# Performance work log

Hardware: AMD Instinct MI355X
Metric: run time of the kernel (lower is better)

## Reference

```python
import jax, jax.numpy as jnp
import numpy as np

N, E = 50000, 400000
IN, HID, OUT = 256, 192, 128  # hidden = floor((128+256)/2) = 192


def setup_inputs() -> dict:
    key = jax.random.key(0)
    ks = jax.random.split(key, 8)
    def glorot(k, fi, fo):
        lim = (6.0 / (fi + fo)) ** 0.5
        return jax.random.uniform(k, (fi, fo), jnp.float32, -lim, lim)
    return {
        "x": jax.random.normal(ks[0], (N, IN), jnp.float32),
        "edge_index": jax.random.randint(ks[1], (2, E), 0, N, jnp.int64),
        "W1": glorot(ks[2], IN, HID),  "b1": jnp.zeros((HID,), jnp.float32),
        "W2": glorot(ks[3], HID, HID), "b2": jnp.zeros((HID,), jnp.float32),
        "W3": glorot(ks[4], HID, OUT), "b3": jnp.zeros((OUT,), jnp.float32),
    }


def gcn_conv(x, src, dst, norm, W, b, n):
    # PyG GCNConv: out = D^-1/2 (A+I) D^-1/2 (x W) + b
    h = x @ W                               # [N, Fout]
    msg = h[src] * norm[:, None]            # [E+N, Fout] gathered, normalized messages
    return jax.ops.segment_sum(msg, dst, num_segments=n) + b


def reference(x, edge_index, W1, b1, W2, b2, W3, b3):
    n = x.shape[0]
    loops = jnp.arange(n, dtype=edge_index.dtype)
    src = jnp.concatenate([edge_index[0], loops])  # add self-loops
    dst = jnp.concatenate([edge_index[1], loops])
    deg = jax.ops.segment_sum(jnp.ones_like(dst, dtype=x.dtype), dst, num_segments=n)
    dinv = jnp.where(deg > 0, deg ** -0.5, 0.0)
    norm = dinv[src] * dinv[dst]            # [E+N]

    h = jax.nn.relu(gcn_conv(x, src, dst, norm, W1, b1, n))
    h = jax.nn.relu(gcn_conv(h, src, dst, norm, W2, b2, n))
    h = jax.nn.sigmoid(gcn_conv(h, src, dst, norm, W3, b3, n))
    # vectorized replacement of the per-element Python threshold loop
    h_clone = jnp.where(h >= 0.5, 1.0, 0.0).astype(h.dtype)
    return h, h_clone
```

## Files before the change

kernel.cpp:

```cpp
#include <hip/hip_runtime.h>
#include <math.h>

constexpr int Nn   = 50000;
constexpr int Ee   = 400000;
constexpr int FIN  = 256;
constexpr int FHID = 192;
constexpr int FOUT = 128;

typedef float    f32x4 __attribute__((ext_vector_type(4)));
typedef _Float16 f16x8 __attribute__((ext_vector_type(8)));

__device__ inline f32x4 mfma16(f16x8 a, f16x8 b, f32x4 c) {
    return __builtin_amdgcn_mfma_f32_16x16x32_f16(a, b, c, 0, 0, 0);
}


__global__ void init_cnt_k(int* cnt, int n) {
    int i = blockIdx.x * blockDim.x + threadIdx.x;
    if (i < n) cnt[i] = 0;
}

__global__ void detect_k(const long long* p, int n, int* flag) {
    if (threadIdx.x == 0 && blockIdx.x == 0) {
        int ok = 1;
        for (int i = 0; i < 16; i++) {
            long long v = p[i];
            if (v < 0 || v >= n) ok = 0;
        }
        *flag = ok;
    }
}

__global__ void conv_k(const void* edge, const int* flag, int* srcI, int* dstI,
                       int* cnt, int ne) {
    int e = blockIdx.x * blockDim.x + threadIdx.x;
    if (e >= ne) return;
    int s, d;
    if (*flag) {
        const long long* p = (const long long*)edge;
        s = (int)p[e];
        d = (int)p[ne + e];
    } else {
        const int* p = (const int*)edge;
        s = p[e];
        d = p[ne + e];
    }
    srcI[e] = s;
    dstI[e] = d;
    atomicAdd(&cnt[d], 1);
}

__global__ void dinv_k(const int* cnt, float* dinv, int n) {
    int i = blockIdx.x * blockDim.x + threadIdx.x;
    if (i < n) dinv[i] = 1.0f / sqrtf((float)(cnt[i] + 1));
}

__global__ __launch_bounds__(256) void scan1_k(const int* cnt, int n, int* rowptr,
                                               int* blockSum) {
    __shared__ int sm[256];
    int b = blockIdx.x, tid = threadIdx.x;
    int gbase = b * 1024 + tid * 4;
    int v[4];
#pragma unroll
    for (int j = 0; j < 4; j++) v[j] = (gbase + j < n) ? cnt[gbase + j] : 0;
    int tsum = v[0] + v[1] + v[2] + v[3];
    sm[tid] = tsum;
    __syncthreads();
    for (int off = 1; off < 256; off <<= 1) {
        int t = (tid >= off) ? sm[tid - off] : 0;
        __syncthreads();
        sm[tid] += t;
        __syncthreads();
    }
    int excl = sm[tid] - tsum;
#pragma unroll
    for (int j = 0; j < 4; j++) {
        if (gbase + j < n) rowptr[gbase + j] = excl;
        excl += v[j];
    }
    if (tid == 255) blockSum[b] = sm[255];
}

__global__ void scan2_k(const int* blockSum, int nb, int* blockOff) {
    if (threadIdx.x == 0 && blockIdx.x == 0) {
        int run = 0;
        for (int b = 0; b < nb; b++) { blockOff[b] = run; run += blockSum[b]; }
        blockOff[nb] = run;
    }
}

__global__ void scan3_k(int* rowptr, const int* blockOff, int* cursor, int n, int nb) {
    int i = blockIdx.x * blockDim.x + threadIdx.x;
    if (i < n) {
        int r = rowptr[i] + blockOff[i >> 10];
        rowptr[i] = r;
        cursor[i] = r;
    }
    if (i == 0) rowptr[n] = blockOff[nb];
}

__global__ void place_k(const int* srcI, const int* dstI, const float* dinv,
                        int* cursor, int* esrc, float* enorm, int ne) {
    int e = blockIdx.x * blockDim.x + threadIdx.x;
    if (e >= ne) return;
    int s = srcI[e], d = dstI[e];
    int pos = atomicAdd(&cursor[d], 1);
    esrc[pos] = s;
    enorm[pos] = dinv[s] * dinv[d];
}

__global__ void split_w_k(const float* __restrict__ W, _Float16* __restrict__ wh,
                          _Float16* __restrict__ wl, int K, int F) {
    int idx = blockIdx.x * blockDim.x + threadIdx.x;
    if (idx >= K * F) return;
    int k = idx / F, f = idx - k * F;
    float w = W[idx];
    _Float16 h = (_Float16)w;
    float d = w - (float)h;
    wh[(size_t)f * K + k] = h;
    wl[(size_t)f * K + k] = (_Float16)(d * 4096.f);
}

template <int NR, int MODE>
struct KSet {
    f16x8  bh[NR], bl[NR];
    f16x8  ah[2], al[2];
    float4 ar[2][2];
};

template <int K, int F, int NR, int MODE>
__device__ inline void load_set(KSet<NR, MODE>& S, int kk,
                                const float* __restrict__ inF,
                                const _Float16* __restrict__ inH,
                                const _Float16* __restrict__ inL,
                                const _Float16* __restrict__ whi,
                                const _Float16* __restrict__ wlo,
                                int r0, int r1, int cb, int l15) {
#pragma unroll
    for (int ni = 0; ni < NR; ni++) {
        const size_t boff = (size_t)(cb + ni * 16 + l15) * K + kk;
        S.bh[ni] = *(const f16x8*)(whi + boff);
        S.bl[ni] = *(const f16x8*)(wlo + boff);
    }
    if constexpr (MODE == 0) {
        const float* p0 = inF + (size_t)r0 * K + kk;
        const float* p1 = inF + (size_t)r1 * K + kk;
        S.ar[0][0] = *(const float4*)p0;
        S.ar[0][1] = *(const float4*)(p0 + 4);
        S.ar[1][0] = *(const float4*)p1;
        S.ar[1][1] = *(const float4*)(p1 + 4);
    } else {
        S.ah[0] = *(const f16x8*)(inH + (size_t)r0 * K + kk);
        S.al[0] = *(const f16x8*)(inL + (size_t)r0 * K + kk);
        S.ah[1] = *(const f16x8*)(inH + (size_t)r1 * K + kk);
        S.al[1] = *(const f16x8*)(inL + (size_t)r1 * K + kk);
    }
}

__device__ inline void split8(float4 f0, float4 f1, f16x8& h, f16x8& l) {
    float v[8] = {f0.x, f0.y, f0.z, f0.w, f1.x, f1.y, f1.z, f1.w};
#pragma unroll
    for (int j = 0; j < 8; j++) {
        _Float16 hh = (_Float16)v[j];
        h[j] = hh;
        l[j] = (_Float16)((v[j] - (float)hh) * 4096.f);
    }
}

template <int NR, int MODE>
__device__ inline void consume_set(KSet<NR, MODE>& S, f32x4 (&accH)[2][NR],
                                   f32x4 (&accL)[2][NR]) {
    f16x8 ah[2], al[2];
    if constexpr (MODE == 0) {
        split8(S.ar[0][0], S.ar[0][1], ah[0], al[0]);
        split8(S.ar[1][0], S.ar[1][1], ah[1], al[1]);
    } else {
        ah[0] = S.ah[0]; al[0] = S.al[0];
        ah[1] = S.ah[1]; al[1] = S.al[1];
    }
#pragma unroll
    for (int ni = 0; ni < NR; ni++)
#pragma unroll
        for (int mi = 0; mi < 2; mi++) {
            accH[mi][ni] = mfma16(ah[mi], S.bh[ni], accH[mi][ni]);
            accL[mi][ni] = mfma16(ah[mi], S.bl[ni], accL[mi][ni]);
            accL[mi][ni] = mfma16(al[mi], S.bh[ni], accL[mi][ni]);
        }
}

template <int K, int F, int NR, int MODE>
__global__ __launch_bounds__(256) void gemm_v2(
    const float* __restrict__ inF, const _Float16* __restrict__ inH,
    const _Float16* __restrict__ inL, const _Float16* __restrict__ whi,
    const _Float16* __restrict__ wlo, float* __restrict__ out, int M) {
    const int tid  = threadIdx.x;
    const int lane = tid & 63;
    const int l15  = lane & 15;
    const int l4   = lane >> 4;
    const int wid  = tid >> 6;
    const int wrow = wid >> 1, wcol = wid & 1;
    const int rb   = blockIdx.x * 64 + wrow * 32;
    const int cb   = (blockIdx.y * 2 + wcol) * (NR * 16);
    const int r0 = min(rb + l15, M - 1);
    const int r1 = min(rb + 16 + l15, M - 1);
    const int kbase = l4 * 8;

    f32x4 accH[2][NR], accL[2][NR];
#pragma unroll
    for (int mi = 0; mi < 2; mi++)
#pragma unroll
        for (int ni = 0; ni < NR; ni++)
#pragma unroll
            for (int r = 0; r < 4; r++) { accH[mi][ni][r] = 0.f; accL[mi][ni][r] = 0.f; }

    KSet<NR, MODE> S0, S1;
    load_set<K, F, NR, MODE>(S0, kbase, inF, inH, inL, whi, wlo, r0, r1, cb, l15);
    for (int k0 = 0; k0 < K; k0 += 64) {
        const int ka = (k0 + 32 < K) ? k0 + 32 : 0;
        load_set<K, F, NR, MODE>(S1, ka + kbase, inF, inH, inL, whi, wlo, r0, r1, cb, l15);
        consume_set<NR, MODE>(S0, accH, accL);
        const int kb = (k0 + 64 < K) ? k0 + 64 : 0;
        load_set<K, F, NR, MODE>(S0, kb + kbase, inF, inH, inL, whi, wlo, r0, r1, cb, l15);
        consume_set<NR, MODE>(S1, accH, accL);
    }

#pragma unroll
    for (int mi = 0; mi < 2; mi++)
#pragma unroll
        for (int r = 0; r < 4; r++) {
            const int row = rb + mi * 16 + l4 * 4 + r;
            if (row < M) {
#pragma unroll
                for (int ni = 0; ni < NR; ni++) {
                    const int col = cb + ni * 16 + l15;
                    out[(size_t)row * F + col] =
                        accH[mi][ni][r] + accL[mi][ni][r] * (1.f / 4096.f);
                }
            }
        }
}

template <int F, int WS>
__global__ void agg2_k(const float* __restrict__ h, const float* __restrict__ dinv,
                       const int* __restrict__ rowptr, const int* __restrict__ esrc,
                       const float* __restrict__ enorm, const float* __restrict__ bias,
                       _Float16* __restrict__ ah, _Float16* __restrict__ al,
                       float* __restrict__ outh, float* __restrict__ outc, int n) {
    constexpr int FV = F / 64;
    int i = (blockIdx.x * blockDim.x + threadIdx.x) >> 6;
    int lane = threadIdx.x & 63;
    if (i >= n) return;
    float di = dinv[i];
    const float* hrow = h + (size_t)i * F;
    float acc[FV];
#pragma unroll
    for (int j = 0; j < FV; j++) acc[j] = di * di * hrow[lane + 64 * j];
    const int e1 = rowptr[i + 1];
    int e = rowptr[i];
    for (; e + 4 <= e1; e += 4) {
        int s0 = esrc[e], s1 = esrc[e + 1], s2 = esrc[e + 2], s3 = esrc[e + 3];
        float w0 = enorm[e], w1 = enorm[e + 1], w2 = enorm[e + 2], w3 = enorm[e + 3];
        const float* p0 = h + (size_t)s0 * F;
        const float* p1 = h + (size_t)s1 * F;
        const float* p2 = h + (size_t)s2 * F;
        const float* p3 = h + (size_t)s3 * F;
#pragma unroll
        for (int j = 0; j < FV; j++) {
            int c = lane + 64 * j;
            float v0 = p0[c], v1 = p1[c], v2 = p2[c], v3 = p3[c];
            acc[j] += w0 * v0;
            acc[j] += w1 * v1;
            acc[j] += w2 * v2;
            acc[j] += w3 * v3;
        }
    }
    for (; e < e1; e++) {
        int s = esrc[e];
        float w = enorm[e];
        const float* hs = h + (size_t)s * F;
#pragma unroll
        for (int j = 0; j < FV; j++) acc[j] += w * hs[lane + 64 * j];
    }
#pragma unroll
    for (int j = 0; j < FV; j++) {
        int c = lane + 64 * j;
        if constexpr (WS == 1) {
            float a = fmaxf(acc[j] + bias[c], 0.f);
            _Float16 hh = (_Float16)a;
            float d = a - (float)hh;
            ah[(size_t)i * F + c] = hh;
            al[(size_t)i * F + c] = (_Float16)(d * 4096.f);
        } else {
            float s = 1.f / (1.f + expf(-(acc[j] + bias[c])));
            outh[(size_t)i * F + c] = s;
            outc[(size_t)i * F + c] = (s >= 0.5f) ? 1.f : 0.f;
        }
    }
}

extern "C" void kernel_launch(void* const* d_in, const int* in_sizes, int n_in,
                              void* d_out, int out_size, void* d_ws, size_t ws_size,
                              hipStream_t stream) {
    const float* x  = (const float*)d_in[0];
    const void*  ei = d_in[1];
    const float* W1 = (const float*)d_in[2];
    const float* b1 = (const float*)d_in[3];
    const float* W2 = (const float*)d_in[4];
    const float* b2 = (const float*)d_in[5];
    const float* W3 = (const float*)d_in[6];
    const float* b3 = (const float*)d_in[7];
    float* out = (float*)d_out;

    char* w = (char*)d_ws;
    size_t off = 0;
    auto alloc = [&](size_t bytes) -> void* {
        off = (off + 255) & ~(size_t)255;
        void* p = w + off;
        off += bytes;
        return p;
    };
    float*     bufA = (float*)alloc((size_t)Nn * FHID * 4);
    _Float16*  Ph   = (_Float16*)alloc((size_t)Nn * FHID * 2);
    _Float16*  Pl   = (_Float16*)alloc((size_t)Nn * FHID * 2);
    int*   srcI   = (int*)alloc((size_t)Ee * 4);
    int*   dstI   = (int*)alloc((size_t)Ee * 4);
    int*   esrc   = (int*)alloc((size_t)Ee * 4);
    float* enorm  = (float*)alloc((size_t)Ee * 4);
    int*   cnt    = (int*)alloc((size_t)Nn * 4);
    float* dinv   = (float*)alloc((size_t)Nn * 4);
    int*   rowptr = (int*)alloc((size_t)(Nn + 1) * 4);
    int*   cursor = (int*)alloc((size_t)Nn * 4);
    int*   blockSum = (int*)alloc(64 * 4);
    int*   blockOff = (int*)alloc(65 * 4);
    int*   flag   = (int*)alloc(4);
    _Float16* w1h = (_Float16*)alloc((size_t)FIN * FHID * 2);
    _Float16* w1l = (_Float16*)alloc((size_t)FIN * FHID * 2);
    _Float16* w2h = (_Float16*)alloc((size_t)FHID * FHID * 2);
    _Float16* w2l = (_Float16*)alloc((size_t)FHID * FHID * 2);
    _Float16* w3h = (_Float16*)alloc((size_t)FHID * FOUT * 2);
    _Float16* w3l = (_Float16*)alloc((size_t)FHID * FOUT * 2);

    const int NB = (Nn + 1023) / 1024;
    const int gN = (Nn + 255) / 256;
    const int gE = (Ee + 255) / 256;

    init_cnt_k<<<gN, 256, 0, stream>>>(cnt, Nn);
    detect_k<<<1, 64, 0, stream>>>((const long long*)ei, Nn, flag);
    conv_k<<<gE, 256, 0, stream>>>(ei, flag, srcI, dstI, cnt, Ee);
    dinv_k<<<gN, 256, 0, stream>>>(cnt, dinv, Nn);
    scan1_k<<<NB, 256, 0, stream>>>(cnt, Nn, rowptr, blockSum);
    scan2_k<<<1, 64, 0, stream>>>(blockSum, NB, blockOff);
    scan3_k<<<gN, 256, 0, stream>>>(rowptr, blockOff, cursor, Nn, NB);
    place_k<<<gE, 256, 0, stream>>>(srcI, dstI, dinv, cursor, esrc, enorm, Ee);

    split_w_k<<<(FIN * FHID + 255) / 256, 256, 0, stream>>>(W1, w1h, w1l, FIN, FHID);
    split_w_k<<<(FHID * FHID + 255) / 256, 256, 0, stream>>>(W2, w2h, w2l, FHID, FHID);
    split_w_k<<<(FHID * FOUT + 255) / 256, 256, 0, stream>>>(W3, w3h, w3l, FHID, FOUT);

    const int gRows = (Nn + 63) / 64;
    const int gAgg  = (Nn * 64 + 255) / 256;

    gemm_v2<FIN, FHID, 3, 0><<<dim3(gRows, 2), 256, 0, stream>>>(
        x, nullptr, nullptr, w1h, w1l, bufA, Nn);
    agg2_k<FHID, 1><<<gAgg, 256, 0, stream>>>(bufA, dinv, rowptr, esrc, enorm,
                                              b1, Ph, Pl, nullptr, nullptr, Nn);
    gemm_v2<FHID, FHID, 3, 2><<<dim3(gRows, 2), 256, 0, stream>>>(
        nullptr, Ph, Pl, w2h, w2l, bufA, Nn);
    agg2_k<FHID, 1><<<gAgg, 256, 0, stream>>>(bufA, dinv, rowptr, esrc, enorm,
                                              b2, Ph, Pl, nullptr, nullptr, Nn);
    gemm_v2<FHID, FOUT, 2, 2><<<dim3(gRows, 2), 256, 0, stream>>>(
        nullptr, Ph, Pl, w3h, w3l, bufA, Nn);
    agg2_k<FOUT, 0><<<gAgg, 256, 0, stream>>>(bufA, dinv, rowptr, esrc, enorm,
                                              b3, nullptr, nullptr, out,
                                              out + (size_t)Nn * FOUT, Nn);
}
```

Measured before the change: 460.9 us.

## Pre-pack weights and hidden activations into MFMA fragment-tiled layout

```diff
diff --git a/kernel.cpp b/kernel.cpp
--- a/kernel.cpp
+++ b/kernel.cpp
@@ -6,6 +6,7 @@
 constexpr int FIN  = 256;
 constexpr int FHID = 192;
 constexpr int FOUT = 128;
+constexpr int MP   = 50048;
 
 typedef float    f32x4 __attribute__((ext_vector_type(4)));
 typedef _Float16 f16x8 __attribute__((ext_vector_type(8)));
@@ -13,6 +14,7 @@
 __device__ inline f32x4 mfma16(f16x8 a, f16x8 b, f32x4 c) {
     return __builtin_amdgcn_mfma_f32_16x16x32_f16(a, b, c, 0, 0, 0);
 }
+
 
 
 __global__ void init_cnt_k(int* cnt, int n) {
@@ -109,90 +111,44 @@
     enorm[pos] = dinv[s] * dinv[d];
 }
 
-__global__ void split_w_k(const float* __restrict__ W, _Float16* __restrict__ wh,
-                          _Float16* __restrict__ wl, int K, int F) {
+__global__ void split_w_pack(const float* __restrict__ W, _Float16* __restrict__ wh,
+                             _Float16* __restrict__ wl, int K, int F) {
     int idx = blockIdx.x * blockDim.x + threadIdx.x;
     if (idx >= K * F) return;
     int k = idx / F, f = idx - k * F;
     float w = W[idx];
     _Float16 h = (_Float16)w;
     float d = w - (float)h;
-    wh[(size_t)f * K + k] = h;
-    wl[(size_t)f * K + k] = (_Float16)(d * 4096.f);
+    int U = (((f >> 4) * (K >> 5) + (k >> 5)) * 4 + ((k >> 3) & 3)) * 16 + (f & 15);
+    size_t off = (size_t)U * 8 + (k & 7);
+    wh[off] = h;
+    wl[off] = (_Float16)(d * 4096.f);
+}
+
+__device__ inline void split8(float4 f0, float4 f1, f16x8& h, f16x8& l) {
+    float v[8] = {f0.x, f0.y, f0.z, f0.w, f1.x, f1.y, f1.z, f1.w};
+#pragma unroll
+    for (int j = 0; j < 8; j++) {
+        _Float16 hh = (_Float16)v[j];
+        h[j] = hh;
+        l[j] = (_Float16)((v[j] - (float)hh) * 4096.f);
+    }
 }
 
 template <int NR, int MODE>
-struct KSet {
+struct Set3 {
     f16x8  bh[NR], bl[NR];
     f16x8  ah[2], al[2];
     float4 ar[2][2];
 };
 
 template <int K, int F, int NR, int MODE>
-__device__ inline void load_set(KSet<NR, MODE>& S, int kk,
-                                const float* __restrict__ inF,
-                                const _Float16* __restrict__ inH,
-                                const _Float16* __restrict__ inL,
-                                const _Float16* __restrict__ whi,
-                                const _Float16* __restrict__ wlo,
-                                int r0, int r1, int cb, int l15) {
-#pragma unroll
-    for (int ni = 0; ni < NR; ni++) {
-        const size_t boff = (size_t)(cb + ni * 16 + l15) * K + kk;
-        S.bh[ni] = *(const f16x8*)(whi + boff);
-        S.bl[ni] = *(const f16x8*)(wlo + boff);
-    }
-    if constexpr (MODE == 0) {
-        const float* p0 = inF + (size_t)r0 * K + kk;
-        const float* p1 = inF + (size_t)r1 * K + kk;
-        S.ar[0][0] = *(const float4*)p0;
-        S.ar[0][1] = *(const float4*)(p0 + 4);
-        S.ar[1][0] = *(const float4*)p1;
-        S.ar[1][1] = *(const float4*)(p1 + 4);
-    } else {
-        S.ah[0] = *(const f16x8*)(inH + (size_t)r0 * K + kk);
-        S.al[0] = *(const f16x8*)(inL + (size_t)r0 * K + kk);
-        S.ah[1] = *(const f16x8*)(inH + (size_t)r1 * K + kk);
-        S.al[1] = *(const f16x8*)(inL + (size_t)r1 * K + kk);
-    }
-}
-
-__device__ inline void split8(float4 f0, float4 f1, f16x8& h, f16x8& l) {
-    float v[8] = {f0.x, f0.y, f0.z, f0.w, f1.x, f1.y, f1.z, f1.w};
-#pragma unroll
-    for (int j = 0; j < 8; j++) {
-        _Float16 hh = (_Float16)v[j];
-        h[j] = hh;
-        l[j] = (_Float16)((v[j] - (float)hh) * 4096.f);
-    }
-}
-
-template <int NR, int MODE>
-__device__ inline void consume_set(KSet<NR, MODE>& S, f32x4 (&accH)[2][NR],
-                                   f32x4 (&accL)[2][NR]) {
-    f16x8 ah[2], al[2];
-    if constexpr (MODE == 0) {
-        split8(S.ar[0][0], S.ar[0][1], ah[0], al[0]);
-        split8(S.ar[1][0], S.ar[1][1], ah[1], al[1]);
-    } else {
-        ah[0] = S.ah[0]; al[0] = S.al[0];
-        ah[1] = S.ah[1]; al[1] = S.al[1];
-    }
-#pragma unroll
-    for (int ni = 0; ni < NR; ni++)
-#pragma unroll
-        for (int mi = 0; mi < 2; mi++) {
-            accH[mi][ni] = mfma16(ah[mi], S.bh[ni], accH[mi][ni]);
-            accL[mi][ni] = mfma16(ah[mi], S.bl[ni], accL[mi][ni]);
-            accL[mi][ni] = mfma16(al[mi], S.bh[ni], accL[mi][ni]);
-        }
-}
-
-template <int K, int F, int NR, int MODE>
-__global__ __launch_bounds__(256) void gemm_v2(
-    const float* __restrict__ inF, const _Float16* __restrict__ inH,
-    const _Float16* __restrict__ inL, const _Float16* __restrict__ whi,
-    const _Float16* __restrict__ wlo, float* __restrict__ out, int M) {
+__global__ __launch_bounds__(256) void gemm_v3(
+    const float* __restrict__ inF,
+    const _Float16* __restrict__ aHp, const _Float16* __restrict__ aLp,
+    const _Float16* __restrict__ bHp, const _Float16* __restrict__ bLp,
+    float* __restrict__ out, int M) {
+    constexpr int KS = K / 32;
     const int tid  = threadIdx.x;
     const int lane = tid & 63;
     const int l15  = lane & 15;
@@ -201,9 +157,14 @@
     const int wrow = wid >> 1, wcol = wid & 1;
     const int rb   = blockIdx.x * 64 + wrow * 32;
     const int cb   = (blockIdx.y * 2 + wcol) * (NR * 16);
+    const int rblk0 = rb >> 4;
+    const int cblk0 = cb >> 4;
+    const f16x8* aH = (const f16x8*)aHp;
+    const f16x8* aL = (const f16x8*)aLp;
+    const f16x8* bH = (const f16x8*)bHp;
+    const f16x8* bL = (const f16x8*)bLp;
     const int r0 = min(rb + l15, M - 1);
     const int r1 = min(rb + 16 + l15, M - 1);
-    const int kbase = l4 * 8;
 
     f32x4 accH[2][NR], accL[2][NR];
 #pragma unroll
@@ -213,15 +174,56 @@
 #pragma unroll
             for (int r = 0; r < 4; r++) { accH[mi][ni][r] = 0.f; accL[mi][ni][r] = 0.f; }
 
-    KSet<NR, MODE> S0, S1;
-    load_set<K, F, NR, MODE>(S0, kbase, inF, inH, inL, whi, wlo, r0, r1, cb, l15);
-    for (int k0 = 0; k0 < K; k0 += 64) {
-        const int ka = (k0 + 32 < K) ? k0 + 32 : 0;
-        load_set<K, F, NR, MODE>(S1, ka + kbase, inF, inH, inL, whi, wlo, r0, r1, cb, l15);
-        consume_set<NR, MODE>(S0, accH, accL);
-        const int kb = (k0 + 64 < K) ? k0 + 64 : 0;
-        load_set<K, F, NR, MODE>(S0, kb + kbase, inF, inH, inL, whi, wlo, r0, r1, cb, l15);
-        consume_set<NR, MODE>(S1, accH, accL);
+    auto load_set = [&](Set3<NR, MODE>& S, int ks) {
+#pragma unroll
+        for (int ni = 0; ni < NR; ni++) {
+            const int b = ((cblk0 + ni) * KS + ks) * 64 + lane;
+            S.bh[ni] = bH[b];
+            S.bl[ni] = bL[b];
+        }
+        if constexpr (MODE == 0) {
+            const int kk = ks * 32 + l4 * 8;
+            const float* p0 = inF + (size_t)r0 * K + kk;
+            const float* p1 = inF + (size_t)r1 * K + kk;
+            S.ar[0][0] = *(const float4*)p0;
+            S.ar[0][1] = *(const float4*)(p0 + 4);
+            S.ar[1][0] = *(const float4*)p1;
+            S.ar[1][1] = *(const float4*)(p1 + 4);
+        } else {
+#pragma unroll
+            for (int mi = 0; mi < 2; mi++) {
+                const int a = ((rblk0 + mi) * KS + ks) * 64 + lane;
+                S.ah[mi] = aH[a];
+                S.al[mi] = aL[a];
+            }
+        }
+    };
+    auto consume_set = [&](Set3<NR, MODE>& S) {
+        f16x8 ah[2], al[2];
+        if constexpr (MODE == 0) {
+            split8(S.ar[0][0], S.ar[0][1], ah[0], al[0]);
+            split8(S.ar[1][0], S.ar[1][1], ah[1], al[1]);
+        } else {
+            ah[0] = S.ah[0]; al[0] = S.al[0];
+            ah[1] = S.ah[1]; al[1] = S.al[1];
+        }
+#pragma unroll
+        for (int ni = 0; ni < NR; ni++)
+#pragma unroll
+            for (int mi = 0; mi < 2; mi++) {
+                accH[mi][ni] = mfma16(ah[mi], S.bh[ni], accH[mi][ni]);
+                accL[mi][ni] = mfma16(ah[mi], S.bl[ni], accL[mi][ni]);
+                accL[mi][ni] = mfma16(al[mi], S.bh[ni], accL[mi][ni]);
+            }
+    };
+
+    Set3<NR, MODE> S0, S1;
+    load_set(S0, 0);
+    for (int ks = 0; ks < KS; ks += 2) {
+        load_set(S1, ks + 1);
+        consume_set(S0);
+        load_set(S0, (ks + 2 < KS) ? ks + 2 : 0);
+        consume_set(S1);
     }
 
 #pragma unroll
@@ -288,8 +290,10 @@
             float a = fmaxf(acc[j] + bias[c], 0.f);
             _Float16 hh = (_Float16)a;
             float d = a - (float)hh;
-            ah[(size_t)i * F + c] = hh;
-            al[(size_t)i * F + c] = (_Float16)(d * 4096.f);
+            int U = (((i >> 4) * (F >> 5) + (c >> 5)) * 4 + ((c >> 3) & 3)) * 16 + (i & 15);
+            size_t off = (size_t)U * 8 + (c & 7);
+            ah[off] = hh;
+            al[off] = (_Float16)(d * 4096.f);
         } else {
             float s = 1.f / (1.f + expf(-(acc[j] + bias[c])));
             outh[(size_t)i * F + c] = s;
@@ -320,8 +324,8 @@
         return p;
     };
     float*     bufA = (float*)alloc((size_t)Nn * FHID * 4);
-    _Float16*  Ph   = (_Float16*)alloc((size_t)Nn * FHID * 2);
-    _Float16*  Pl   = (_Float16*)alloc((size_t)Nn * FHID * 2);
+    _Float16*  Ph   = (_Float16*)alloc((size_t)MP * FHID * 2);
+    _Float16*  Pl   = (_Float16*)alloc((size_t)MP * FHID * 2);
     int*   srcI   = (int*)alloc((size_t)Ee * 4);
     int*   dstI   = (int*)alloc((size_t)Ee * 4);
     int*   esrc   = (int*)alloc((size_t)Ee * 4);
@@ -353,22 +357,22 @@
     scan3_k<<<gN, 256, 0, stream>>>(rowptr, blockOff, cursor, Nn, NB);
     place_k<<<gE, 256, 0, stream>>>(srcI, dstI, dinv, cursor, esrc, enorm, Ee);
 
-    split_w_k<<<(FIN * FHID + 255) / 256, 256, 0, stream>>>(W1, w1h, w1l, FIN, FHID);
-    split_w_k<<<(FHID * FHID + 255) / 256, 256, 0, stream>>>(W2, w2h, w2l, FHID, FHID);
-    split_w_k<<<(FHID * FOUT + 255) / 256, 256, 0, stream>>>(W3, w3h, w3l, FHID, FOUT);
-
-    const int gRows = (Nn + 63) / 64;
+    split_w_pack<<<(FIN * FHID + 255) / 256, 256, 0, stream>>>(W1, w1h, w1l, FIN, FHID);
+    split_w_pack<<<(FHID * FHID + 255) / 256, 256, 0, stream>>>(W2, w2h, w2l, FHID, FHID);
+    split_w_pack<<<(FHID * FOUT + 255) / 256, 256, 0, stream>>>(W3, w3h, w3l, FHID, FOUT);
+
+    const int gRows = MP / 64;
     const int gAgg  = (Nn * 64 + 255) / 256;
 
-    gemm_v2<FIN, FHID, 3, 0><<<dim3(gRows, 2), 256, 0, stream>>>(
+    gemm_v3<FIN, FHID, 3, 0><<<dim3(gRows, 2), 256, 0, stream>>>(
         x, nullptr, nullptr, w1h, w1l, bufA, Nn);
     agg2_k<FHID, 1><<<gAgg, 256, 0, stream>>>(bufA, dinv, rowptr, esrc, enorm,
                                               b1, Ph, Pl, nullptr, nullptr, Nn);
-    gemm_v2<FHID, FHID, 3, 2><<<dim3(gRows, 2), 256, 0, stream>>>(
+    gemm_v3<FHID, FHID, 3, 2><<<dim3(gRows, 2), 256, 0, stream>>>(
         nullptr, Ph, Pl, w2h, w2l, bufA, Nn);
     agg2_k<FHID, 1><<<gAgg, 256, 0, stream>>>(bufA, dinv, rowptr, esrc, enorm,
                                               b2, Ph, Pl, nullptr, nullptr, Nn);
-    gemm_v2<FHID, FOUT, 2, 2><<<dim3(gRows, 2), 256, 0, stream>>>(
+    gemm_v3<FHID, FOUT, 2, 2><<<dim3(gRows, 2), 256, 0, stream>>>(
         nullptr, Ph, Pl, w3h, w3l, bufA, Nn);
     agg2_k<FOUT, 0><<<gAgg, 256, 0, stream>>>(bufA, dinv, rowptr, esrc, enorm,
                                               b3, nullptr, nullptr, out,
```

After: 405.5 us. 1.14x faster.
